# Kernel tuning notes

Hardware: AMD Instinct MI355X
Metric: run time of the kernel (lower is better)

Reference implementation:

```python
import jax, jax.numpy as jnp
import numpy as np

B, S, H = 8, 2048, 256

def setup_inputs() -> dict:
    key = jax.random.key(0)
    ks = jax.random.split(key, 7)
    sc = 0.05
    return {
        "inputs": jax.random.normal(ks[0], (B, S, H), dtype=jnp.float32),
        "Wq": jax.random.normal(ks[1], (H, H), dtype=jnp.float32) * sc,
        "bq": jax.random.normal(ks[2], (H,), dtype=jnp.float32) * sc,
        "Wk": jax.random.normal(ks[3], (H, H), dtype=jnp.float32) * sc,
        "bk": jax.random.normal(ks[4], (H,), dtype=jnp.float32) * sc,
        "Wv": jax.random.normal(ks[5], (H, H), dtype=jnp.float32) * sc,
        "bv": jax.random.normal(ks[6], (H,), dtype=jnp.float32) * sc,
    }

def reference(inputs, Wq, bq, Wk, bk, Wv, bv):
    # nn.Linear: y = x @ W.T + b
    q = jnp.einsum("bsh,oh->bso", inputs, Wq) + bq
    k = jnp.einsum("bsh,oh->bso", inputs, Wk) + bk
    v = jnp.einsum("bsh,oh->bso", inputs, Wv) + bv
    hidden = q.shape[-1]
    # NOTE: original scales by sqrt(hidden^2) == hidden (not sqrt(hidden))
    scores = jnp.einsum("bqh,bkh->bqk", q, k) / jnp.float32(hidden)
    # NOTE: original applies softmax over dim=1 (the query axis), not the last axis
    weights = jax.nn.softmax(scores, axis=1)
    return jnp.einsum("bqk,bkh->bqh", weights, v)
```

## Files before the change

### kernel.cpp

```cpp
#include <hip/hip_runtime.h>
#include <hip/hip_bf16.h>

#define B_ 8
#define S_ 2048
#define H_ 256
#define BS_ (B_*S_)

typedef __attribute__((ext_vector_type(8))) short bf16x8;
typedef __attribute__((ext_vector_type(4))) short bf16x4;
typedef __attribute__((ext_vector_type(4))) float f32x4;

static __device__ inline short f2bf(float f) {
  union { float f; unsigned int u; } a; a.f = f;
  unsigned int u = a.u;
  unsigned int r = (u + 0x7fffu + ((u >> 16) & 1u)) >> 16;
  return (short)r;
}

static __device__ inline float bf2f(short s) {
  union { float f; unsigned int u; } a;
  a.u = ((unsigned int)(unsigned short)s) << 16;
  return a.f;
}

static __device__ inline f32x4 mfma16(bf16x8 a, bf16x8 b, f32x4 c) {
  return __builtin_amdgcn_mfma_f32_16x16x32_bf16(a, b, c, 0, 0, 0);
}

static __device__ inline void gl_lds16(const short* g, short* l) {
  __builtin_amdgcn_global_load_lds(
      (const __attribute__((address_space(1))) void*)g,
      (__attribute__((address_space(3))) void*)l, 16, 0, 0);
}

#define NX4 (BS_ * H_ / 4)
#define NW4 (H_ * H_ / 4)
#define NTOT4 (NX4 + 3 * NW4)
#define NALL4 (NTOT4 + BS_ / 4)

__global__ __launch_bounds__(256) void cvt_bf16(
    const float* __restrict__ x,
    const float* __restrict__ Wq, const float* __restrict__ Wk,
    const float* __restrict__ Wv,
    short* __restrict__ xb, short* __restrict__ wqb,
    short* __restrict__ wkb, short* __restrict__ wvb,
    float* __restrict__ den)
{
  int stride = gridDim.x * blockDim.x;
  for (int i = blockIdx.x * blockDim.x + threadIdx.x; i < NALL4; i += stride) {
    if (i >= NTOT4) {
      float4 z = {0.f, 0.f, 0.f, 0.f};
      *(float4*)(den + (size_t)(i - NTOT4) * 4) = z;
      continue;
    }
    const float* src; short* dst; int off;
    if (i < NX4) { src = x; dst = xb; off = i; }
    else {
      int j = i - NX4;
      int w = j >> 14;
      off = j & (NW4 - 1);
      src = (w == 0) ? Wq : (w == 1) ? Wk : Wv;
      dst = (w == 0) ? wqb : (w == 1) ? wkb : wvb;
    }
    float4 v = *(const float4*)(src + off * 4);
    bf16x4 p;
    p[0] = f2bf(v.x); p[1] = f2bf(v.y); p[2] = f2bf(v.z); p[3] = f2bf(v.w);
    *(bf16x4*)(dst + off * 4) = p;
  }
}

__global__ __launch_bounds__(256) void qkv_proj(
    const short* __restrict__ x,
    const short* __restrict__ Wq, const float* __restrict__ bq,
    const short* __restrict__ Wk, const float* __restrict__ bk,
    const short* __restrict__ Wv, const float* __restrict__ bv,
    short* __restrict__ Qo, short* __restrict__ Ko, short* __restrict__ VTo)
{
  const int tid  = threadIdx.x;
  const int wave = tid >> 6;
  const int lane = tid & 63;
  const int quad = lane >> 4;
  const int l16  = lane & 15;
  const int y    = blockIdx.y;

  const short* W    = (y == 0) ? Wq : (y == 1) ? Wk : Wv;
  const float* bias = (y == 0) ? bq : (y == 1) ? bk : bv;
  const int sblk = blockIdx.x * 64;

  __shared__ short wbuf[16 * 512];
  __shared__ short xbuf[4 * 512];

  f32x4 zero = {0.f, 0.f, 0.f, 0.f};
  f32x4 acc[4][4];
#pragma unroll
  for (int i = 0; i < 4; i++)
#pragma unroll
    for (int j = 0; j < 4; j++) acc[i][j] = zero;

  for (int ch = 0; ch < 8; ch++) {
#pragma unroll
    for (int i = 0; i < 4; i++) {
      int r = wave * 4 + i;
      gl_lds16(W + (r * 16 + l16) * H_ + ch * 32 + quad * 8, wbuf + r * 512);
    }
    gl_lds16(x + (sblk + wave * 16 + l16) * H_ + ch * 32 + quad * 8,
             xbuf + wave * 512);
    __syncthreads();
    bf16x8 af[4];
#pragma unroll
    for (int st = 0; st < 4; st++)
      af[st] = *(const bf16x8*)(xbuf + st * 512 + lane * 8);
#pragma unroll
    for (int i = 0; i < 4; i++) {
      bf16x8 bb = *(const bf16x8*)(wbuf + (wave * 4 + i) * 512 + lane * 8);
#pragma unroll
      for (int st = 0; st < 4; st++)
        acc[st][i] = mfma16(af[st], bb, acc[st][i]);
    }
    __syncthreads();
  }

  if (y < 2) {
    short* dst = (y == 0) ? Qo : Ko;
#pragma unroll
    for (int i = 0; i < 4; i++) {
      int col = (wave * 4 + i) * 16 + l16;
      float bvl = bias[col];
#pragma unroll
      for (int st = 0; st < 4; st++) {
#pragma unroll
        for (int r = 0; r < 4; r++) {
          int row = sblk + st * 16 + quad * 4 + r;
          dst[row * H_ + col] = f2bf(acc[st][i][r] + bvl);
        }
      }
    }
  } else {
#pragma unroll
    for (int i = 0; i < 4; i++) {
      int col = (wave * 4 + i) * 16 + l16;
      float bvl = bias[col];
#pragma unroll
      for (int st = 0; st < 4; st++) {
        int row0  = sblk + st * 16 + quad * 4;
        int b_idx = row0 >> 11;
        int k0    = row0 & (S_ - 1);
        bf16x4 pk;
#pragma unroll
        for (int r = 0; r < 4; r++) pk[r] = f2bf(acc[st][i][r] + bvl);
        *(bf16x4*)(VTo + (size_t)b_idx * H_ * S_ + (size_t)col * S_ + k0) = pk;
      }
    }
  }
}

__global__ __launch_bounds__(256) void scores(
    const short* __restrict__ Q, const short* __restrict__ K,
    short* __restrict__ Pf, float* __restrict__ den)
{
  const int tid  = threadIdx.x;
  const int wave = tid >> 6;
  const int lane = tid & 63;
  const int quad = lane >> 4;
  const int l16  = lane & 15;
  const int bx = ((blockIdx.x & 7) << 8) | (blockIdx.x >> 3);
  const int qt = bx & 15;
  const int kt = (bx >> 4) & 15;
  const int b  = bx >> 8;

  const short* Qb = Q + b * S_ * H_;
  const short* Kb = K + b * S_ * H_;

  const int krow0 = kt * 128 + wave * 32;
  const int qcol0 = qt * 128;
  const int kw    = krow0 >> 5;

  __shared__ short qbuf[64 * 512];

  bf16x8 kreg[2][8];
  const short* kbase = Kb + (krow0 + l16) * H_ + quad * 8;
#pragma unroll
  for (int kf = 0; kf < 2; kf++)
#pragma unroll
    for (int ch = 0; ch < 8; ch++)
      kreg[kf][ch] = *(const bf16x8*)(kbase + kf * 16 * H_ + ch * 32);

#pragma unroll
  for (int i = 0; i < 16; i++) {
    int region = wave * 16 + i;
    int qf = region >> 3;
    int ch = region & 7;
    gl_lds16(Qb + (qcol0 + qf * 16 + l16) * H_ + ch * 32 + quad * 8,
             qbuf + region * 512);
  }
  __syncthreads();

  f32x4 zero = {0.f, 0.f, 0.f, 0.f};
  f32x4 acc[2][8];
#pragma unroll
  for (int i = 0; i < 2; i++)
#pragma unroll
    for (int j = 0; j < 8; j++) acc[i][j] = zero;

#pragma unroll
  for (int ch = 0; ch < 8; ch++) {
#pragma unroll
    for (int qf = 0; qf < 8; qf++) {
      bf16x8 bq = *(const bf16x8*)(qbuf + (qf * 8 + ch) * 512 + lane * 8);
      acc[0][qf] = mfma16(kreg[0][ch], bq, acc[0][qf]);
      acc[1][qf] = mfma16(kreg[1][ch], bq, acc[1][qf]);
    }
  }

  const int quadA = quad >> 1;
  const int j0    = (quad & 1) * 4;
  float rs[2][4] = {{0.f,0.f,0.f,0.f},{0.f,0.f,0.f,0.f}};
#pragma unroll
  for (int kf = 0; kf < 2; kf++) {
#pragma unroll
    for (int qf = 0; qf < 8; qf++) {
      bf16x4 pk;
#pragma unroll
      for (int r = 0; r < 4; r++) {
        float e = __expf(acc[kf][qf][r] * (1.0f / H_));
        rs[kf][r] += e;
        pk[r] = f2bf(e);
      }
      size_t tile = ((size_t)(b * 128 + qt * 8 + qf) << 6) + kw;
      *(bf16x4*)(Pf + (tile << 9) + ((2 * kf + quadA) * 16 + l16) * 8 + j0) = pk;
    }
  }

#pragma unroll
  for (int kf = 0; kf < 2; kf++) {
#pragma unroll
    for (int r = 0; r < 4; r++) {
      float v = rs[kf][r];
      v += __shfl_xor(v, 1, 64);
      v += __shfl_xor(v, 2, 64);
      v += __shfl_xor(v, 4, 64);
      v += __shfl_xor(v, 8, 64);
      if (l16 == 0)
        atomicAdd(&den[b * S_ + krow0 + kf * 16 + quad * 4 + r], v);
    }
  }
}

__global__ __launch_bounds__(256) void vscale(
    short* __restrict__ VT, const float* __restrict__ den)
{
  int i = blockIdx.x * 256 + threadIdx.x;
  int b  = i >> 17;
  int k0 = (i & 511) << 2;
  float4 df = *(const float4*)(den + b * S_ + k0);
  bf16x4 v = *(bf16x4*)(VT + (size_t)i * 4);
  bf16x4 o;
  o[0] = f2bf(bf2f(v[0]) / df.x);
  o[1] = f2bf(bf2f(v[1]) / df.y);
  o[2] = f2bf(bf2f(v[2]) / df.z);
  o[3] = f2bf(bf2f(v[3]) / df.w);
  *(bf16x4*)(VT + (size_t)i * 4) = o;
}

__global__ __launch_bounds__(256) void pv(
    const short* __restrict__ Pf, const short* __restrict__ VTs,
    float* __restrict__ out)
{
  const int tid  = threadIdx.x;
  const int wave = tid >> 6;
  const int lane = tid & 63;
  const int quad = lane >> 4;
  const int l16  = lane & 15;
  const int bx = blockIdx.x;
  const int qt = bx >> 4;
  const int b  = (bx >> 1) & 7;
  const int hs = bx & 1;

  __shared__ short vbuf[32 * 512];
  __shared__ short abuf[16 * 512];

  const int qt16 = qt * 4 + wave;
  const short* VTb = VTs + (size_t)b * H_ * S_ + (size_t)(hs * 128) * S_;
  const size_t tilebase = ((size_t)(b * 128 + qt16) * 64) << 9;

  f32x4 zero = {0.f, 0.f, 0.f, 0.f};
  f32x4 acc[8];
#pragma unroll
  for (int i = 0; i < 8; i++) acc[i] = zero;

  for (int kc = 0; kc < S_; kc += 128) {
#pragma unroll
    for (int i = 0; i < 8; i++) {
      int id = wave * 8 + i;
      int n  = id >> 2;
      int kw = id & 3;
      const short* g = VTb + (size_t)(n * 16 + l16) * S_ + kc + kw * 32 + quad * 8;
      gl_lds16(g, vbuf + id * 512);
    }
#pragma unroll
    for (int kwi = 0; kwi < 4; kwi++) {
      const short* g = Pf + tilebase + (size_t)((kc >> 5) + kwi) * 512 + lane * 8;
      gl_lds16(g, abuf + (wave * 4 + kwi) * 512);
    }
    __syncthreads();
#pragma unroll
    for (int kw = 0; kw < 4; kw++) {
      bf16x8 a = *(const bf16x8*)(abuf + (wave * 4 + kw) * 512 + lane * 8);
#pragma unroll
      for (int n = 0; n < 8; n++) {
        bf16x8 vb = *(const bf16x8*)(vbuf + (n * 4 + kw) * 512 + lane * 8);
        acc[n] = mfma16(a, vb, acc[n]);
      }
    }
    __syncthreads();
  }

  const int q0 = qt16 * 16;
#pragma unroll
  for (int n = 0; n < 8; n++) {
    int col = hs * 128 + n * 16 + l16;
#pragma unroll
    for (int r = 0; r < 4; r++) {
      int q = q0 + quad * 4 + r;
      out[((size_t)b * S_ + q) * H_ + col] = acc[n][r];
    }
  }
}

extern "C" void kernel_launch(void* const* d_in, const int* in_sizes, int n_in,
                              void* d_out, int out_size, void* d_ws, size_t ws_size,
                              hipStream_t stream) {
  const float* x  = (const float*)d_in[0];
  const float* Wq = (const float*)d_in[1];
  const float* bq = (const float*)d_in[2];
  const float* Wk = (const float*)d_in[3];
  const float* bk = (const float*)d_in[4];
  const float* Wv = (const float*)d_in[5];
  const float* bv = (const float*)d_in[6];

  short* xb  = (short*)d_ws;
  short* wqb = xb  + (size_t)BS_ * H_;
  short* wkb = wqb + H_ * H_;
  short* wvb = wkb + H_ * H_;
  short* Qs  = wvb + H_ * H_;
  short* Ks  = Qs  + (size_t)BS_ * H_;
  short* VT  = Ks  + (size_t)BS_ * H_;
  short* P   = VT  + (size_t)BS_ * H_;
  float* den = (float*)(P + (size_t)B_ * S_ * S_);
  float* outp = (float*)d_out;

  cvt_bf16<<<1024, 256, 0, stream>>>(x, Wq, Wk, Wv, xb, wqb, wkb, wvb, den);
  qkv_proj<<<dim3(BS_ / 64, 3), 256, 0, stream>>>(xb, wqb, bq, wkb, bk, wvb, bv, Qs, Ks, VT);
  scores<<<2048, 256, 0, stream>>>(Qs, Ks, P, den);
  vscale<<<4096, 256, 0, stream>>>(VT, den);
  pv<<<512, 256, 0, stream>>>(P, VT, outp);
}
```

Baseline: 191.5 us.

## Reuse LDS Q tile across four K tiles per block with prefetched K registers

```diff
diff --git a/kernel.cpp b/kernel.cpp
--- a/kernel.cpp
+++ b/kernel.cpp
@@ -154,7 +154,7 @@
   }
 }
 
-__global__ __launch_bounds__(256) void scores(
+__global__ __launch_bounds__(256, 2) void scores(
     const short* __restrict__ Q, const short* __restrict__ K,
     short* __restrict__ Pf, float* __restrict__ den)
 {
@@ -163,27 +163,25 @@
   const int lane = tid & 63;
   const int quad = lane >> 4;
   const int l16  = lane & 15;
-  const int bx = ((blockIdx.x & 7) << 8) | (blockIdx.x >> 3);
-  const int qt = bx & 15;
-  const int kt = (bx >> 4) & 15;
-  const int b  = bx >> 8;
+  const int ktg = blockIdx.x & 3;
+  const int qt  = (blockIdx.x >> 2) & 15;
+  const int b   = blockIdx.x >> 6;
 
   const short* Qb = Q + b * S_ * H_;
   const short* Kb = K + b * S_ * H_;
-
-  const int krow0 = kt * 128 + wave * 32;
   const int qcol0 = qt * 128;
-  const int kw    = krow0 >> 5;
 
   __shared__ short qbuf[64 * 512];
 
-  bf16x8 kreg[2][8];
-  const short* kbase = Kb + (krow0 + l16) * H_ + quad * 8;
-#pragma unroll
-  for (int kf = 0; kf < 2; kf++)
-#pragma unroll
-    for (int ch = 0; ch < 8; ch++)
-      kreg[kf][ch] = *(const bf16x8*)(kbase + kf * 16 * H_ + ch * 32);
+  bf16x8 kreg[2][2][8];
+  {
+    const short* kb = Kb + ((ktg * 4) * 128 + wave * 32 + l16) * H_ + quad * 8;
+#pragma unroll
+    for (int kf = 0; kf < 2; kf++)
+#pragma unroll
+      for (int ch = 0; ch < 8; ch++)
+        kreg[0][kf][ch] = *(const bf16x8*)(kb + kf * 16 * H_ + ch * 32);
+  }
 
 #pragma unroll
   for (int i = 0; i < 16; i++) {
@@ -195,53 +193,70 @@
   }
   __syncthreads();
 
-  f32x4 zero = {0.f, 0.f, 0.f, 0.f};
-  f32x4 acc[2][8];
-#pragma unroll
-  for (int i = 0; i < 2; i++)
-#pragma unroll
-    for (int j = 0; j < 8; j++) acc[i][j] = zero;
-
-#pragma unroll
-  for (int ch = 0; ch < 8; ch++) {
-#pragma unroll
-    for (int qf = 0; qf < 8; qf++) {
-      bf16x8 bq = *(const bf16x8*)(qbuf + (qf * 8 + ch) * 512 + lane * 8);
-      acc[0][qf] = mfma16(kreg[0][ch], bq, acc[0][qf]);
-      acc[1][qf] = mfma16(kreg[1][ch], bq, acc[1][qf]);
-    }
-  }
-
   const int quadA = quad >> 1;
   const int j0    = (quad & 1) * 4;
-  float rs[2][4] = {{0.f,0.f,0.f,0.f},{0.f,0.f,0.f,0.f}};
-#pragma unroll
-  for (int kf = 0; kf < 2; kf++) {
-#pragma unroll
-    for (int qf = 0; qf < 8; qf++) {
-      bf16x4 pk;
+
+#pragma unroll
+  for (int t = 0; t < 4; t++) {
+    if (t < 3) {
+      const short* kb = Kb + ((ktg * 4 + t + 1) * 128 + wave * 32 + l16) * H_ + quad * 8;
+#pragma unroll
+      for (int kf = 0; kf < 2; kf++)
+#pragma unroll
+        for (int ch = 0; ch < 8; ch++)
+          kreg[(t + 1) & 1][kf][ch] = *(const bf16x8*)(kb + kf * 16 * H_ + ch * 32);
+    }
+
+    f32x4 zero = {0.f, 0.f, 0.f, 0.f};
+    f32x4 acc[2][8];
+#pragma unroll
+    for (int i = 0; i < 2; i++)
+#pragma unroll
+      for (int j = 0; j < 8; j++) acc[i][j] = zero;
+
+#pragma unroll
+    for (int ch = 0; ch < 8; ch++) {
+#pragma unroll
+      for (int qf = 0; qf < 8; qf++) {
+        bf16x8 bq = *(const bf16x8*)(qbuf + (qf * 8 + ch) * 512 + lane * 8);
+        acc[0][qf] = mfma16(kreg[t & 1][0][ch], bq, acc[0][qf]);
+        acc[1][qf] = mfma16(kreg[t & 1][1][ch], bq, acc[1][qf]);
+      }
+    }
+
+    const int kt    = ktg * 4 + t;
+    const int krow0 = kt * 128 + wave * 32;
+    const int kw    = krow0 >> 5;
+
+    float rs[2][4] = {{0.f,0.f,0.f,0.f},{0.f,0.f,0.f,0.f}};
+#pragma unroll
+    for (int kf = 0; kf < 2; kf++) {
+#pragma unroll
+      for (int qf = 0; qf < 8; qf++) {
+        bf16x4 pk;
+#pragma unroll
+        for (int r = 0; r < 4; r++) {
+          float e = __expf(acc[kf][qf][r] * (1.0f / H_));
+          rs[kf][r] += e;
+          pk[r] = f2bf(e);
+        }
+        size_t tile = ((size_t)(b * 128 + qt * 8 + qf) << 6) + kw;
+        *(bf16x4*)(Pf + (tile << 9) + ((2 * kf + quadA) * 16 + l16) * 8 + j0) = pk;
+      }
+    }
+
+#pragma unroll
+    for (int kf = 0; kf < 2; kf++) {
 #pragma unroll
       for (int r = 0; r < 4; r++) {
-        float e = __expf(acc[kf][qf][r] * (1.0f / H_));
-        rs[kf][r] += e;
-        pk[r] = f2bf(e);
-      }
-      size_t tile = ((size_t)(b * 128 + qt * 8 + qf) << 6) + kw;
-      *(bf16x4*)(Pf + (tile << 9) + ((2 * kf + quadA) * 16 + l16) * 8 + j0) = pk;
-    }
-  }
-
-#pragma unroll
-  for (int kf = 0; kf < 2; kf++) {
-#pragma unroll
-    for (int r = 0; r < 4; r++) {
-      float v = rs[kf][r];
-      v += __shfl_xor(v, 1, 64);
-      v += __shfl_xor(v, 2, 64);
-      v += __shfl_xor(v, 4, 64);
-      v += __shfl_xor(v, 8, 64);
-      if (l16 == 0)
-        atomicAdd(&den[b * S_ + krow0 + kf * 16 + quad * 4 + r], v);
+        float v = rs[kf][r];
+        v += __shfl_xor(v, 1, 64);
+        v += __shfl_xor(v, 2, 64);
+        v += __shfl_xor(v, 4, 64);
+        v += __shfl_xor(v, 8, 64);
+        if (l16 == 0)
+          atomicAdd(&den[b * S_ + krow0 + kf * 16 + quad * 4 + r], v);
+      }
     }
   }
 }
@@ -351,7 +366,7 @@
 
   cvt_bf16<<<1024, 256, 0, stream>>>(x, Wq, Wk, Wv, xb, wqb, wkb, wvb, den);
   qkv_proj<<<dim3(BS_ / 64, 3), 256, 0, stream>>>(xb, wqb, bq, wkb, bk, wvb, bv, Qs, Ks, VT);
-  scores<<<2048, 256, 0, stream>>>(Qs, Ks, P, den);
+  scores<<<512, 256, 0, stream>>>(Qs, Ks, P, den);
   vscale<<<4096, 256, 0, stream>>>(VT, den);
   pv<<<512, 256, 0, stream>>>(P, VT, outp);
 }
```

Result: faster. 185.1 us, median of 3 (-3.4%).
